# Performance work log

Measured on AMD Instinct MI355X. Metric: run time of the kernel, lower is better.

## Reference

```python
import jax, jax.numpy as jnp
import numpy as np

HIDDEN = 128
EDGE_DIM = 32
N_NODES = 50000
N_EDGES = 800000


def setup_inputs() -> dict:
    key = jax.random.key(0)
    ks = jax.random.split(key, 8)
    node_features = jax.random.normal(ks[0], (N_NODES, HIDDEN), dtype=jnp.float32)
    edge_index = jax.random.randint(ks[1], (2, N_EDGES), 0, N_NODES, dtype=jnp.int64)
    edge_attr = jax.random.normal(ks[2], (N_EDGES, EDGE_DIM), dtype=jnp.float32)
    # parameters (Linear stored as [in, out] for x @ W + b)
    s_et = 1.0 / np.sqrt(EDGE_DIM)
    W_edge = jax.random.uniform(ks[3], (EDGE_DIM, HIDDEN), jnp.float32, -s_et, s_et)
    b_edge = jnp.zeros((HIDDEN,), jnp.float32)
    s1 = 1.0 / np.sqrt(3 * HIDDEN)
    W1 = jax.random.uniform(ks[4], (3 * HIDDEN, HIDDEN), jnp.float32, -s1, s1)
    b1 = jnp.zeros((HIDDEN,), jnp.float32)
    s2 = 1.0 / np.sqrt(HIDDEN)
    W2 = jax.random.uniform(ks[5], (HIDDEN, 1), jnp.float32, -s2, s2)
    b2 = jnp.zeros((1,), jnp.float32)
    return {
        "node_features": node_features,
        "edge_attr": edge_attr,
        "W_edge": W_edge, "b_edge": b_edge,
        "W1": W1, "b1": b1, "W2": W2, "b2": b2,
        "edge_index": edge_index,
    }


def reference(node_features, edge_attr, W_edge, b_edge, W1, b1, W2, b2, edge_index):
    row, col = edge_index[0], edge_index[1]
    src = node_features[row]                 # [E, H] gather
    dst = node_features[col]                 # [E, H] gather
    edge_feat = edge_attr @ W_edge + b_edge  # [E, H]
    combined = jnp.concatenate([src, edge_feat, dst], axis=-1)  # [E, 3H]
    h = jax.nn.relu(combined @ W1 + b1)      # [E, H]
    attn = jax.nn.sigmoid(h @ W2 + b2)       # [E, 1]
    return attn
```

## Files before the change

kernel.cpp:

```cpp
#include <hip/hip_runtime.h>
#include <hip/hip_bf16.h>

#define HIDDEN   128
#define EDGE_DIM 32
#define NNODE    50000
#define NEDGE    800000
#define KSTEPS   9
#define NFRAG    8
#define LDS_KS   8

typedef __attribute__((ext_vector_type(4))) float        f32x4;
typedef __attribute__((ext_vector_type(8))) short        bf16x8;
typedef __attribute__((ext_vector_type(4))) unsigned int u32x4;

#define BPACK_USHORTS  (KSTEPS * NFRAG * 64 * 8)
#define BIAS_OFF_BYTES (BPACK_USHORTS * 2)
#define FLAG_OFF_BYTES (BIAS_OFF_BYTES + 128 * 4)
#define DATA_OFF       74752

#define PP_OFF   DATA_OFF
#define QP_OFF   (PP_OFF + NNODE * HIDDEN * 2)
#define IDXN_OFF (QP_OFF + NNODE * HIDDEN * 2)
#define WS_NEW   (IDXN_OFF + 2 * NEDGE * 4)

#define NODE_OFF_BYTES DATA_OFF
#define IDX_OFF_BYTES  (NODE_OFF_BYTES + NNODE * HIDDEN * 2)
#define WS_R8          (IDX_OFF_BYTES + 2 * NEDGE * 4)

__device__ __forceinline__ unsigned short f2bf(float f) {
  unsigned u = __builtin_bit_cast(unsigned, f);
  u += 0x7FFFu + ((u >> 16) & 1u);
  return (unsigned short)(u >> 16);
}

__device__ __forceinline__ unsigned cvt_pk_bf16(float a, float b) {
  union { __hip_bfloat162 h; unsigned u; } cv;
  cv.h = __float22bfloat162_rn(make_float2(a, b));
  return cv.u;
}

__device__ __forceinline__ bf16x8 pack8(f32x4 lo, f32x4 hi) {
  u32x4 u;
  u[0] = cvt_pk_bf16(lo[0], lo[1]);
  u[1] = cvt_pk_bf16(lo[2], lo[3]);
  u[2] = cvt_pk_bf16(hi[0], hi[1]);
  u[3] = cvt_pk_bf16(hi[2], hi[3]);
  return __builtin_bit_cast(bf16x8, u);
}

__device__ __forceinline__ void gload_lds16(const void* g, void* l) {
  __builtin_amdgcn_global_load_lds(
      (const __attribute__((address_space(1))) unsigned int*)g,
      (__attribute__((address_space(3))) unsigned int*)l, 16, 0, 0);
}

#define MFMA(a, b, c) __builtin_amdgcn_mfma_f32_16x16x32_bf16((a), (b), (c), 0, 0, 0)

__global__ void setup_kernel(const float* __restrict__ W_edge,
                             const float* __restrict__ b_edge,
                             const float* __restrict__ W1,
                             const float* __restrict__ b1,
                             const void*  __restrict__ eidx,
                             unsigned short* __restrict__ Bpack,
                             float* __restrict__ bias_eff,
                             int*   __restrict__ flag64) {
  const int bid = blockIdx.x, tid = threadIdx.x;
  if (bid < 36) {
    const int pair  = bid * 2 + (tid >> 6);
    const int lane  = tid & 63;
    const int kstep = pair >> 3;
    const int f     = pair & 7;
    const int col   = f * 16 + (lane & 15);
    const int kbase = kstep * 32 + (lane >> 4) * 8;
    float vals[8];
#pragma unroll
    for (int j = 0; j < 8; ++j) {
      const int k = kbase + j;
      float val;
      if (k < 128) {
        val = W1[k * 128 + col];
      } else if (k < 256) {
        val = W1[(k + 128) * 128 + col];
      } else {
        const int kk = k - 256;
        float s = 0.f;
        for (int t = 0; t < 128; ++t)
          s = fmaf(W_edge[kk * 128 + t], W1[(128 + t) * 128 + col], s);
        val = s;
      }
      vals[j] = val;
    }
    u32x4 sv;
#pragma unroll
    for (int j = 0; j < 4; ++j)
      sv[j] = (unsigned)f2bf(vals[2 * j]) | ((unsigned)f2bf(vals[2 * j + 1]) << 16);
    *(u32x4*)(Bpack + ((kstep * NFRAG + f) * 64 + lane) * 8) = sv;
  } else {
    if (tid < 128) {
      float s = b1[tid];
      for (int t = 0; t < 128; ++t)
        s = fmaf(b_edge[t], W1[(128 + t) * 128 + tid], s);
      bias_eff[tid] = s;
    }
    if (tid == 0) {
      const unsigned* w = (const unsigned*)eidx;
      int all0 = 1;
      for (int i = 0; i < 64; ++i) all0 &= (w[2 * i + 1] == 0u) ? 1 : 0;
      *flag64 = all0;
    }
  }
}

__global__ __launch_bounds__(256) void cvt_nodes_kernel(const float* __restrict__ nodef,
                                                        unsigned short* __restrict__ nbf) {
  const int i = blockIdx.x * 256 + threadIdx.x;
  if (i >= NNODE * HIDDEN / 8) return;
  f32x4 lo = *(const f32x4*)(nodef + i * 8);
  f32x4 hi = *(const f32x4*)(nodef + i * 8 + 4);
  *(bf16x8*)(nbf + i * 8) = pack8(lo, hi);
}

__global__ __launch_bounds__(256) void cvt_idx_kernel(const void* __restrict__ eidx,
                                                      const int* __restrict__ flag64,
                                                      int* __restrict__ idx32) {
  const int i = blockIdx.x * 256 + threadIdx.x;
  if (i >= 2 * NEDGE) return;
  if (*flag64) idx32[i] = (int)((const long long*)eidx)[i];
  else         idx32[i] = ((const int*)eidx)[i];
}

__global__ __launch_bounds__(512, 2) void pq_kernel(
    const float* __restrict__ nodef,
    const unsigned short* __restrict__ Bpack,
    const float* __restrict__ bias_eff,
    unsigned* __restrict__ Pp,
    unsigned* __restrict__ Qp) {
  __shared__ unsigned short lds_b[LDS_KS * NFRAG * 64 * 8];

  const int tid  = threadIdx.x;
  const int lane = tid & 63;
  const int wid  = tid >> 6;
  const int l15  = lane & 15;
  const int kg   = lane >> 4;
  const int nb   = blockIdx.x * 256 + wid * 32;

#pragma unroll
  for (int i = 0; i < 8; ++i) {
    const char* g = (const char*)Bpack + (size_t)(i * 512 + tid) * 16;
    char*       l = (char*)lds_b + (size_t)(i * 512 + wid * 64) * 16;
    gload_lds16(g, l);
  }

  const int n0 = min(nb + l15, NNODE - 1);
  const int n1 = min(nb + 16 + l15, NNODE - 1);
  bf16x8 a0[4], a1[4];
#pragma unroll
  for (int ks = 0; ks < 4; ++ks) {
    const float* p0 = nodef + (size_t)n0 * HIDDEN + ks * 32 + kg * 8;
    const float* p1 = nodef + (size_t)n1 * HIDDEN + ks * 32 + kg * 8;
    a0[ks] = pack8(*(const f32x4*)p0, *(const f32x4*)(p0 + 4));
    a1[ks] = pack8(*(const f32x4*)p1, *(const f32x4*)(p1 + 4));
  }

  float bv[NFRAG];
#pragma unroll
  for (int f = 0; f < NFRAG; ++f) bv[f] = bias_eff[f * 16 + l15];

  __syncthreads();

  f32x4 acc[2][NFRAG];
#pragma unroll
  for (int m = 0; m < 2; ++m)
#pragma unroll
    for (int f = 0; f < NFRAG; ++f)
      acc[m][f] = (f32x4){bv[f], bv[f], bv[f], bv[f]};
#pragma unroll
  for (int ks = 0; ks < 4; ++ks)
#pragma unroll
    for (int f = 0; f < NFRAG; ++f) {
      bf16x8 bfr = *(const bf16x8*)(lds_b + ((ks * NFRAG + f) * 64 + lane) * 8);
      acc[0][f] = MFMA(a0[ks], bfr, acc[0][f]);
      acc[1][f] = MFMA(a1[ks], bfr, acc[1][f]);
    }
#pragma unroll
  for (int m = 0; m < 2; ++m)
#pragma unroll
    for (int r = 0; r < 4; ++r) {
      const int n = nb + m * 16 + kg * 4 + r;
      if (n < NNODE) {
#pragma unroll
        for (int k = 0; k < 4; ++k)
          Pp[(size_t)n * 64 + k * 16 + l15] =
              cvt_pk_bf16(acc[m][2 * k][r], acc[m][2 * k + 1][r]);
      }
    }

#pragma unroll
  for (int m = 0; m < 2; ++m)
#pragma unroll
    for (int f = 0; f < NFRAG; ++f)
      acc[m][f] = (f32x4){0.f, 0.f, 0.f, 0.f};
#pragma unroll
  for (int ks = 0; ks < 4; ++ks)
#pragma unroll
    for (int f = 0; f < NFRAG; ++f) {
      bf16x8 bfr = *(const bf16x8*)(lds_b + (((ks + 4) * NFRAG + f) * 64 + lane) * 8);
      acc[0][f] = MFMA(a0[ks], bfr, acc[0][f]);
      acc[1][f] = MFMA(a1[ks], bfr, acc[1][f]);
    }
#pragma unroll
  for (int m = 0; m < 2; ++m)
#pragma unroll
    for (int r = 0; r < 4; ++r) {
      const int n = nb + m * 16 + kg * 4 + r;
      if (n < NNODE) {
#pragma unroll
        for (int k = 0; k < 4; ++k)
          Qp[(size_t)n * 64 + k * 16 + l15] =
              cvt_pk_bf16(acc[m][2 * k][r], acc[m][2 * k + 1][r]);
      }
    }
}

__global__ __launch_bounds__(256, 3) void edge_attn_pq(
    const float* __restrict__ eattr,
    const int*   __restrict__ idx32,
    const unsigned* __restrict__ Pp,
    const unsigned* __restrict__ Qp,
    const unsigned short* __restrict__ Bpack,
    const float* __restrict__ W2,
    const float* __restrict__ b2,
    float* __restrict__ out) {
  const int tid   = threadIdx.x;
  const int lane  = tid & 63;
  const int wid   = tid >> 6;
  const int l15   = lane & 15;
  const int kg    = lane >> 4;
  const int ebase = blockIdx.x * 128 + wid * 32;

  const f32x4 zero4 = {0.f, 0.f, 0.f, 0.f};

  int rn[2][4], cn[2][4];
#pragma unroll
  for (int m = 0; m < 2; ++m)
#pragma unroll
    for (int r = 0; r < 4; ++r) {
      rn[m][r] = idx32[ebase + m * 16 + kg * 4 + r];
      cn[m][r] = idx32[NEDGE + ebase + m * 16 + kg * 4 + r];
    }

  bf16x8 ae0, ae1;
  {
    const float* pe = eattr + (size_t)(ebase + l15) * EDGE_DIM + kg * 8;
    ae0 = pack8(*(const f32x4*)pe, *(const f32x4*)(pe + 4));
  }
  {
    const float* pe = eattr + (size_t)(ebase + 16 + l15) * EDGE_DIM + kg * 8;
    ae1 = pack8(*(const f32x4*)pe, *(const f32x4*)(pe + 4));
  }

  f32x4 acc[2][NFRAG];
#pragma unroll
  for (int f = 0; f < NFRAG; ++f) {
    bf16x8 bfr = *(const bf16x8*)(Bpack + ((8 * NFRAG + f) * 64 + lane) * 8);
    acc[0][f] = MFMA(ae0, bfr, zero4);
    acc[1][f] = MFMA(ae1, bfr, zero4);
  }

  unsigned pu[2][4][4], qu[2][4][4];
#pragma unroll
  for (int m = 0; m < 2; ++m)
#pragma unroll
    for (int r = 0; r < 4; ++r) {
      const unsigned* pb = Pp + (size_t)rn[m][r] * 64 + l15;
      const unsigned* qb = Qp + (size_t)cn[m][r] * 64 + l15;
#pragma unroll
      for (int k = 0; k < 4; ++k) {
        pu[m][r][k] = pb[k * 16];
        qu[m][r][k] = qb[k * 16];
      }
    }

#pragma unroll
  for (int m = 0; m < 2; ++m)
#pragma unroll
    for (int r = 0; r < 4; ++r)
#pragma unroll
      for (int k = 0; k < 4; ++k) {
        const unsigned up = pu[m][r][k], uq = qu[m][r][k];
        acc[m][2 * k][r]     += __builtin_bit_cast(float, up << 16)
                              + __builtin_bit_cast(float, uq << 16);
        acc[m][2 * k + 1][r] += __builtin_bit_cast(float, up & 0xffff0000u)
                              + __builtin_bit_cast(float, uq & 0xffff0000u);
      }

  float w2v[NFRAG];
#pragma unroll
  for (int f = 0; f < NFRAG; ++f) w2v[f] = W2[f * 16 + l15];
  const float bias2 = b2[0];

  float part[2][4];
#pragma unroll
  for (int m = 0; m < 2; ++m)
#pragma unroll
    for (int rr = 0; rr < 4; ++rr) {
      float s = 0.f;
#pragma unroll
      for (int f = 0; f < NFRAG; ++f) {
        float h = fmaxf(acc[m][f][rr], 0.f);
        s = fmaf(h, w2v[f], s);
      }
      part[m][rr] = s;
    }

#pragma unroll
  for (int mask = 1; mask < 16; mask <<= 1)
#pragma unroll
    for (int m = 0; m < 2; ++m)
#pragma unroll
      for (int rr = 0; rr < 4; ++rr)
        part[m][rr] += __shfl_xor(part[m][rr], mask, 64);

  if (l15 == 0) {
#pragma unroll
    for (int m = 0; m < 2; ++m)
#pragma unroll
      for (int rr = 0; rr < 4; ++rr) {
        float x = part[m][rr] + bias2;
        out[ebase + m * 16 + kg * 4 + rr] = 1.f / (1.f + __expf(-x));
      }
  }
}

__global__ __launch_bounds__(512, 4) void edge_attn_kernel(
    const unsigned short* __restrict__ nbf,
    const float* __restrict__ eattr,
    const int*   __restrict__ idx32,
    const unsigned short* __restrict__ Bpack,
    const float* __restrict__ bias_eff,
    const float* __restrict__ W2,
    const float* __restrict__ b2,
    float* __restrict__ out) {
  __shared__ unsigned short lds_b[LDS_KS * NFRAG * 64 * 8];

  const int tid   = threadIdx.x;
  const int lane  = tid & 63;
  const int wid   = tid >> 6;
  const int l15   = lane & 15;
  const int kg    = lane >> 4;
  const int ebase = blockIdx.x * 256 + wid * 32;

#pragma unroll
  for (int i = 0; i < 8; ++i) {
    const char* g = (const char*)Bpack + (size_t)(i * 512 + tid) * 16;
    char*       l = (char*)lds_b + (size_t)(i * 512 + wid * 64) * 16;
    gload_lds16(g, l);
  }

  const int r0 = idx32[ebase + l15];
  const int r1 = idx32[ebase + 16 + l15];
  const int c0 = idx32[NEDGE + ebase + l15];
  const int c1 = idx32[NEDGE + ebase + 16 + l15];

  bf16x8 a0[4], a1[4];
#pragma unroll
  for (int ks = 0; ks < 4; ++ks) {
    a0[ks] = *(const bf16x8*)(nbf + (size_t)r0 * HIDDEN + kg * 8 + ks * 32);
    a1[ks] = *(const bf16x8*)(nbf + (size_t)r1 * HIDDEN + kg * 8 + ks * 32);
  }

  __syncthreads();

  f32x4 acc[2][NFRAG];
#pragma unroll
  for (int m = 0; m < 2; ++m)
#pragma unroll
    for (int f = 0; f < NFRAG; ++f)
      acc[m][f] = (f32x4){0.f, 0.f, 0.f, 0.f};

#pragma unroll
  for (int ks = 0; ks < 4; ++ks)
#pragma unroll
    for (int f = 0; f < NFRAG; ++f) {
      bf16x8 bfr = *(const bf16x8*)(lds_b + ((ks * NFRAG + f) * 64 + lane) * 8);
      acc[0][f] = MFMA(a0[ks], bfr, acc[0][f]);
      acc[1][f] = MFMA(a1[ks], bfr, acc[1][f]);
    }

  __builtin_amdgcn_sched_barrier(0);

#pragma unroll
  for (int ks = 0; ks < 4; ++ks) {
    a0[ks] = *(const bf16x8*)(nbf + (size_t)c0 * HIDDEN + kg * 8 + ks * 32);
    a1[ks] = *(const bf16x8*)(nbf + (size_t)c1 * HIDDEN + kg * 8 + ks * 32);
  }

#pragma unroll
  for (int ks = 0; ks < 4; ++ks)
#pragma unroll
    for (int f = 0; f < NFRAG; ++f) {
      bf16x8 bfr = *(const bf16x8*)(lds_b + (((ks + 4) * NFRAG + f) * 64 + lane) * 8);
      acc[0][f] = MFMA(a0[ks], bfr, acc[0][f]);
      acc[1][f] = MFMA(a1[ks], bfr, acc[1][f]);
    }

  __builtin_amdgcn_sched_barrier(0);

  bf16x8 ae0, ae1;
  {
    const float* pe = eattr + (size_t)(ebase + l15) * EDGE_DIM + kg * 8;
    ae0 = pack8(*(const f32x4*)pe, *(const f32x4*)(pe + 4));
  }
  {
    const float* pe = eattr + (size_t)(ebase + 16 + l15) * EDGE_DIM + kg * 8;
    ae1 = pack8(*(const f32x4*)pe, *(const f32x4*)(pe + 4));
  }
#pragma unroll
  for (int f = 0; f < NFRAG; ++f) {
    bf16x8 bfr = *(const bf16x8*)(Bpack + ((8 * NFRAG + f) * 64 + lane) * 8);
    acc[0][f] = MFMA(ae0, bfr, acc[0][f]);
    acc[1][f] = MFMA(ae1, bfr, acc[1][f]);
  }

  float w2v[NFRAG], bv[NFRAG];
#pragma unroll
  for (int f = 0; f < NFRAG; ++f) {
    w2v[f] = W2[f * 16 + l15];
    bv[f]  = bias_eff[f * 16 + l15];
  }
  const float bias2 = b2[0];

  float part[2][4];
#pragma unroll
  for (int m = 0; m < 2; ++m)
#pragma unroll
    for (int rr = 0; rr < 4; ++rr) {
      float s = 0.f;
#pragma unroll
      for (int f = 0; f < NFRAG; ++f) {
        float h = fmaxf(acc[m][f][rr] + bv[f], 0.f);
        s = fmaf(h, w2v[f], s);
      }
      part[m][rr] = s;
    }

#pragma unroll
  for (int mask = 1; mask < 16; mask <<= 1)
#pragma unroll
    for (int m = 0; m < 2; ++m)
#pragma unroll
      for (int rr = 0; rr < 4; ++rr)
        part[m][rr] += __shfl_xor(part[m][rr], mask, 64);

  if (l15 == 0) {
#pragma unroll
    for (int m = 0; m < 2; ++m)
#pragma unroll
      for (int rr = 0; rr < 4; ++rr) {
        float x = part[m][rr] + bias2;
        out[ebase + m * 16 + kg * 4 + rr] = 1.f / (1.f + __expf(-x));
      }
  }
}

__global__ __launch_bounds__(256) void edge_attn_kernel_fp32(
    const float* __restrict__ nodef,
    const float* __restrict__ eattr,
    const void*  __restrict__ eidx,
    const unsigned short* __restrict__ Bpack,
    const float* __restrict__ bias_eff,
    const float* __restrict__ W2,
    const float* __restrict__ b2,
    const int*   __restrict__ flag64,
    float* __restrict__ out) {
  const int lane  = threadIdx.x & 63;
  const int wid   = threadIdx.x >> 6;
  const int ebase = blockIdx.x * 128 + wid * 32;
  const int l15   = lane & 15;
  const int kg    = lane >> 4;
  const int koff  = kg * 8;
  const int e0 = ebase + l15;
  const int e1 = e0 + 16;

  long r0, c0, r1, c1;
  if (*flag64) {
    const long long* p = (const long long*)eidx;
    r0 = (long)p[e0];          r1 = (long)p[e1];
    c0 = (long)p[NEDGE + e0];  c1 = (long)p[NEDGE + e1];
  } else {
    const int* p = (const int*)eidx;
    r0 = p[e0];          r1 = p[e1];
    c0 = p[NEDGE + e0];  c1 = p[NEDGE + e1];
  }

  f32x4 acc[2][NFRAG];
#pragma unroll
  for (int m = 0; m < 2; ++m)
#pragma unroll
    for (int f = 0; f < NFRAG; ++f)
      acc[m][f] = (f32x4){0.f, 0.f, 0.f, 0.f};

#pragma unroll 1
  for (int ks = 0; ks < KSTEPS; ++ks) {
    const float *p0, *p1;
    if (ks < 4)      { p0 = nodef + r0 * HIDDEN + ks * 32;       p1 = nodef + r1 * HIDDEN + ks * 32; }
    else if (ks < 8) { p0 = nodef + c0 * HIDDEN + (ks - 4) * 32; p1 = nodef + c1 * HIDDEN + (ks - 4) * 32; }
    else             { p0 = eattr + (long)e0 * EDGE_DIM;         p1 = eattr + (long)e1 * EDGE_DIM; }

    f32x4 lo0 = *(const f32x4*)(p0 + koff);
    f32x4 hi0 = *(const f32x4*)(p0 + koff + 4);
    f32x4 lo1 = *(const f32x4*)(p1 + koff);
    f32x4 hi1 = *(const f32x4*)(p1 + koff + 4);
    bf16x8 a0 = pack8(lo0, hi0);
    bf16x8 a1 = pack8(lo1, hi1);

#pragma unroll
    for (int f = 0; f < NFRAG; ++f) {
      bf16x8 bfr = *(const bf16x8*)(Bpack + ((ks * NFRAG + f) * 64 + lane) * 8);
      acc[0][f] = MFMA(a0, bfr, acc[0][f]);
      acc[1][f] = MFMA(a1, bfr, acc[1][f]);
    }
  }

  float w2v[NFRAG], bv[NFRAG];
#pragma unroll
  for (int f = 0; f < NFRAG; ++f) {
    w2v[f] = W2[f * 16 + l15];
    bv[f]  = bias_eff[f * 16 + l15];
  }
  const float bias2 = b2[0];

  float part[2][4];
#pragma unroll
  for (int m = 0; m < 2; ++m)
#pragma unroll
    for (int r = 0; r < 4; ++r) {
      float s = 0.f;
#pragma unroll
      for (int f = 0; f < NFRAG; ++f) {
        float h = acc[m][f][r] + bv[f];
        h = fmaxf(h, 0.f);
        s = fmaf(h, w2v[f], s);
      }
      part[m][r] = s;
    }

#pragma unroll
  for (int mask = 1; mask < 16; mask <<= 1)
#pragma unroll
    for (int m = 0; m < 2; ++m)
#pragma unroll
      for (int r = 0; r < 4; ++r)
        part[m][r] += __shfl_xor(part[m][r], mask, 64);

  if (l15 == 0) {
#pragma unroll
    for (int m = 0; m < 2; ++m)
#pragma unroll
      for (int r = 0; r < 4; ++r) {
        float x = part[m][r] + bias2;
        out[ebase + m * 16 + kg * 4 + r] = 1.f / (1.f + __expf(-x));
      }
  }
}

extern "C" void kernel_launch(void* const* d_in, const int* in_sizes, int n_in,
                              void* d_out, int out_size, void* d_ws, size_t ws_size,
                              hipStream_t stream) {
  const float* nodef  = (const float*)d_in[0];
  const float* eattr  = (const float*)d_in[1];
  const float* W_edge = (const float*)d_in[2];
  const float* b_edge = (const float*)d_in[3];
  const float* W1     = (const float*)d_in[4];
  const float* b1     = (const float*)d_in[5];
  const float* W2     = (const float*)d_in[6];
  const float* b2     = (const float*)d_in[7];
  const void*  eidx   = d_in[8];

  unsigned short* Bpack    = (unsigned short*)d_ws;
  float*          bias_eff = (float*)((char*)d_ws + BIAS_OFF_BYTES);
  int*            flag64   = (int*)((char*)d_ws + FLAG_OFF_BYTES);

  setup_kernel<<<dim3(37), dim3(128), 0, stream>>>(W_edge, b_edge, W1, b1, eidx,
                                                   Bpack, bias_eff, flag64);

  if (ws_size >= (size_t)WS_NEW) {
    unsigned* Pp    = (unsigned*)((char*)d_ws + PP_OFF);
    unsigned* Qp    = (unsigned*)((char*)d_ws + QP_OFF);
    int*      idx32 = (int*)((char*)d_ws + IDXN_OFF);
    cvt_idx_kernel<<<dim3((2 * NEDGE + 255) / 256), dim3(256), 0, stream>>>(eidx, flag64, idx32);
    pq_kernel<<<dim3((NNODE + 255) / 256), dim3(512), 0, stream>>>(nodef, Bpack, bias_eff, Pp, Qp);
    edge_attn_pq<<<dim3(NEDGE / 128), dim3(256), 0, stream>>>(
        eattr, idx32, Pp, Qp, Bpack, W2, b2, (float*)d_out);
  } else if (ws_size >= (size_t)WS_R8) {
    unsigned short* nbf   = (unsigned short*)((char*)d_ws + NODE_OFF_BYTES);
    int*            idx32 = (int*)((char*)d_ws + IDX_OFF_BYTES);
    cvt_idx_kernel<<<dim3((2 * NEDGE + 255) / 256), dim3(256), 0, stream>>>(eidx, flag64, idx32);
    cvt_nodes_kernel<<<dim3((NNODE * HIDDEN / 8 + 255) / 256), dim3(256), 0, stream>>>(nodef, nbf);
    edge_attn_kernel<<<dim3(NEDGE / 256), dim3(512), 0, stream>>>(
        nbf, eattr, idx32, Bpack, bias_eff, W2, b2, (float*)d_out);
  } else {
    edge_attn_kernel_fp32<<<dim3(NEDGE / 128), dim3(256), 0, stream>>>(
        nodef, eattr, eidx, Bpack, bias_eff, W2, b2, flag64, (float*)d_out);
  }
}
```

Measured before the change: 112.9 us.

## Vectorize P/Q gathers with permuted row layout and drop LDS staging in pq_kernel

Rearranges the bf16 P/Q node-projection rows so each lane's four packed values are contiguous. Both the producer stores and the per-edge gathers become single 16-byte accesses instead of four strided 4-byte accesses. The gather loads and the W2 loads are issued before the edge-attribute MFMAs so more latency can be hidden. pq_kernel moves to 256-thread blocks and reads the B fragments straight from global memory instead of staging them through LDS, which removes a barrier but relies on cache hits for B.

```diff
diff --git a/kernel.cpp b/kernel.cpp
--- a/kernel.cpp
+++ b/kernel.cpp
@@ -129,27 +129,18 @@
   else         idx32[i] = ((const int*)eidx)[i];
 }
 
-__global__ __launch_bounds__(512, 2) void pq_kernel(
+__global__ __launch_bounds__(256, 3) void pq_kernel(
     const float* __restrict__ nodef,
     const unsigned short* __restrict__ Bpack,
     const float* __restrict__ bias_eff,
     unsigned* __restrict__ Pp,
     unsigned* __restrict__ Qp) {
-  __shared__ unsigned short lds_b[LDS_KS * NFRAG * 64 * 8];
-
   const int tid  = threadIdx.x;
   const int lane = tid & 63;
   const int wid  = tid >> 6;
   const int l15  = lane & 15;
   const int kg   = lane >> 4;
-  const int nb   = blockIdx.x * 256 + wid * 32;
-
-#pragma unroll
-  for (int i = 0; i < 8; ++i) {
-    const char* g = (const char*)Bpack + (size_t)(i * 512 + tid) * 16;
-    char*       l = (char*)lds_b + (size_t)(i * 512 + wid * 64) * 16;
-    gload_lds16(g, l);
-  }
+  const int nb   = blockIdx.x * 128 + wid * 32;
 
   const int n0 = min(nb + l15, NNODE - 1);
   const int n1 = min(nb + 16 + l15, NNODE - 1);
@@ -166,8 +157,6 @@
 #pragma unroll
   for (int f = 0; f < NFRAG; ++f) bv[f] = bias_eff[f * 16 + l15];
 
-  __syncthreads();
-
   f32x4 acc[2][NFRAG];
 #pragma unroll
   for (int m = 0; m < 2; ++m)
@@ -178,7 +167,7 @@
   for (int ks = 0; ks < 4; ++ks)
 #pragma unroll
     for (int f = 0; f < NFRAG; ++f) {
-      bf16x8 bfr = *(const bf16x8*)(lds_b + ((ks * NFRAG + f) * 64 + lane) * 8);
+      bf16x8 bfr = *(const bf16x8*)(Bpack + ((ks * NFRAG + f) * 64 + lane) * 8);
       acc[0][f] = MFMA(a0[ks], bfr, acc[0][f]);
       acc[1][f] = MFMA(a1[ks], bfr, acc[1][f]);
     }
@@ -188,10 +177,11 @@
     for (int r = 0; r < 4; ++r) {
       const int n = nb + m * 16 + kg * 4 + r;
       if (n < NNODE) {
+        u32x4 sv;
 #pragma unroll
         for (int k = 0; k < 4; ++k)
-          Pp[(size_t)n * 64 + k * 16 + l15] =
-              cvt_pk_bf16(acc[m][2 * k][r], acc[m][2 * k + 1][r]);
+          sv[k] = cvt_pk_bf16(acc[m][2 * k][r], acc[m][2 * k + 1][r]);
+        *(u32x4*)(Pp + (size_t)n * 64 + l15 * 4) = sv;
       }
     }
 
@@ -204,7 +194,7 @@
   for (int ks = 0; ks < 4; ++ks)
 #pragma unroll
     for (int f = 0; f < NFRAG; ++f) {
-      bf16x8 bfr = *(const bf16x8*)(lds_b + (((ks + 4) * NFRAG + f) * 64 + lane) * 8);
+      bf16x8 bfr = *(const bf16x8*)(Bpack + (((ks + 4) * NFRAG + f) * 64 + lane) * 8);
       acc[0][f] = MFMA(a0[ks], bfr, acc[0][f]);
       acc[1][f] = MFMA(a1[ks], bfr, acc[1][f]);
     }
@@ -214,10 +204,11 @@
     for (int r = 0; r < 4; ++r) {
       const int n = nb + m * 16 + kg * 4 + r;
       if (n < NNODE) {
+        u32x4 sv;
 #pragma unroll
         for (int k = 0; k < 4; ++k)
-          Qp[(size_t)n * 64 + k * 16 + l15] =
-              cvt_pk_bf16(acc[m][2 * k][r], acc[m][2 * k + 1][r]);
+          sv[k] = cvt_pk_bf16(acc[m][2 * k][r], acc[m][2 * k + 1][r]);
+        *(u32x4*)(Qp + (size_t)n * 64 + l15 * 4) = sv;
       }
     }
 }
@@ -249,6 +240,18 @@
       cn[m][r] = idx32[NEDGE + ebase + m * 16 + kg * 4 + r];
     }
 
+  u32x4 pu[2][4], qu[2][4];
+#pragma unroll
+  for (int m = 0; m < 2; ++m)
+#pragma unroll
+    for (int r = 0; r < 4; ++r)
+      pu[m][r] = *(const u32x4*)(Pp + (size_t)rn[m][r] * 64 + l15 * 4);
+#pragma unroll
+  for (int m = 0; m < 2; ++m)
+#pragma unroll
+    for (int r = 0; r < 4; ++r)
+      qu[m][r] = *(const u32x4*)(Qp + (size_t)cn[m][r] * 64 + l15 * 4);
+
   bf16x8 ae0, ae1;
   {
     const float* pe = eattr + (size_t)(ebase + l15) * EDGE_DIM + kg * 8;
@@ -259,6 +262,11 @@
     ae1 = pack8(*(const f32x4*)pe, *(const f32x4*)(pe + 4));
   }
 
+  float w2v[NFRAG];
+#pragma unroll
+  for (int f = 0; f < NFRAG; ++f) w2v[f] = W2[f * 16 + l15];
+  const float bias2 = b2[0];
+
   f32x4 acc[2][NFRAG];
 #pragma unroll
   for (int f = 0; f < NFRAG; ++f) {
@@ -267,37 +275,26 @@
     acc[1][f] = MFMA(ae1, bfr, zero4);
   }
 
-  unsigned pu[2][4][4], qu[2][4][4];
-#pragma unroll
-  for (int m = 0; m < 2; ++m)
-#pragma unroll
-    for (int r = 0; r < 4; ++r) {
-      const unsigned* pb = Pp + (size_t)rn[m][r] * 64 + l15;
-      const unsigned* qb = Qp + (size_t)cn[m][r] * 64 + l15;
+#pragma unroll
+  for (int m = 0; m < 2; ++m)
+#pragma unroll
+    for (int r = 0; r < 4; ++r)
 #pragma unroll
       for (int k = 0; k < 4; ++k) {
-        pu[m][r][k] = pb[k * 16];
-        qu[m][r][k] = qb[k * 16];
-      }
-    }
-
+        const unsigned up = pu[m][r][k];
+        acc[m][2 * k][r]     += __builtin_bit_cast(float, up << 16);
+        acc[m][2 * k + 1][r] += __builtin_bit_cast(float, up & 0xffff0000u);
+      }
 #pragma unroll
   for (int m = 0; m < 2; ++m)
 #pragma unroll
     for (int r = 0; r < 4; ++r)
 #pragma unroll
       for (int k = 0; k < 4; ++k) {
-        const unsigned up = pu[m][r][k], uq = qu[m][r][k];
-        acc[m][2 * k][r]     += __builtin_bit_cast(float, up << 16)
-                              + __builtin_bit_cast(float, uq << 16);
-        acc[m][2 * k + 1][r] += __builtin_bit_cast(float, up & 0xffff0000u)
-                              + __builtin_bit_cast(float, uq & 0xffff0000u);
-      }
-
-  float w2v[NFRAG];
-#pragma unroll
-  for (int f = 0; f < NFRAG; ++f) w2v[f] = W2[f * 16 + l15];
-  const float bias2 = b2[0];
+        const unsigned uq = qu[m][r][k];
+        acc[m][2 * k][r]     += __builtin_bit_cast(float, uq << 16);
+        acc[m][2 * k + 1][r] += __builtin_bit_cast(float, uq & 0xffff0000u);
+      }
 
   float part[2][4];
 #pragma unroll
@@ -589,7 +586,7 @@
     unsigned* Qp    = (unsigned*)((char*)d_ws + QP_OFF);
     int*      idx32 = (int*)((char*)d_ws + IDXN_OFF);
     cvt_idx_kernel<<<dim3((2 * NEDGE + 255) / 256), dim3(256), 0, stream>>>(eidx, flag64, idx32);
-    pq_kernel<<<dim3((NNODE + 255) / 256), dim3(512), 0, stream>>>(nodef, Bpack, bias_eff, Pp, Qp);
+    pq_kernel<<<dim3((NNODE + 127) / 128), dim3(256), 0, stream>>>(nodef, Bpack, bias_eff, Pp, Qp);
     edge_attn_pq<<<dim3(NEDGE / 128), dim3(256), 0, stream>>>(
         eattr, idx32, Pp, Qp, Bpack, W2, b2, (float*)d_out);
   } else if (ws_size >= (size_t)WS_R8) {
```

Measured after the change: 117.5 us. 1.04x slower.
